# Optimization experiments

Hardware: AMD Instinct MI355X
Metric: run time of the kernel (lower is better)

The kernel has to match this reference:

```python
import jax, jax.numpy as jnp
import numpy as np

N, E = 50000, 600000
IN_C, HID, OUT_C = 256, 128, 2
R, B, L = 7, 8, 3
ALPHA = 0.1


def _rgcn(x, src, dst, etype, comp, basis, root, bias):
    # comp: [R,B], basis: [B,d,d] -> per-relation weights W: [R,d,d]
    n, d = x.shape
    W = jnp.einsum('rb,bdf->rdf', comp, basis)
    # combined (dst, relation) segment id for per-relation mean aggregation
    seg = dst * R + etype
    msg = x[src]  # [E,d] gather
    s = jax.ops.segment_sum(msg, seg, num_segments=n * R)  # [N*R,d]
    cnt = jax.ops.segment_sum(jnp.ones((E,), x.dtype), seg, num_segments=n * R)
    agg = (s / jnp.maximum(cnt, 1.0)[:, None]).reshape(n, R, d)  # per-relation mean
    return x @ root + bias + jnp.einsum('nrd,rdf->nf', agg, W)


def setup_inputs() -> dict:
    key = jax.random.key(0)
    ks = jax.random.split(key, 10)
    sc = 0.05
    x = jax.random.normal(ks[0], (N, IN_C), dtype=jnp.float32)
    edge_index = jax.random.randint(ks[1], (2, E), 0, N)
    edge_type = jax.random.randint(ks[2], (E,), 0, R)
    # GPR temp init: alpha*(1-alpha)^k, last entry (1-alpha)^K
    temp = jnp.asarray(ALPHA * (1.0 - ALPHA) ** np.arange(L + 1), dtype=jnp.float32)
    temp = temp.at[-1].set((1.0 - ALPHA) ** L)
    lin1_w = jax.random.normal(ks[3], (IN_C, HID), jnp.float32) * sc
    lin1_b = jnp.zeros((HID,), jnp.float32)
    lin2_w = jax.random.normal(ks[4], (HID, OUT_C), jnp.float32) * sc
    lin2_b = jnp.zeros((OUT_C,), jnp.float32)
    comps = jax.random.normal(ks[5], (L, R, B), jnp.float32) * sc
    bases = jax.random.normal(ks[6], (L, B, HID, HID), jnp.float32) * sc
    roots = jax.random.normal(ks[7], (L, HID, HID), jnp.float32) * sc
    conv_biases = jnp.zeros((L, HID), jnp.float32)
    return dict(x=x, edge_index=edge_index, edge_type=edge_type, temp=temp,
                lin1_w=lin1_w, lin1_b=lin1_b, lin2_w=lin2_w, lin2_b=lin2_b,
                comps=comps, bases=bases, roots=roots, conv_biases=conv_biases)


def reference(x, edge_index, edge_type, temp, lin1_w, lin1_b, lin2_w, lin2_b,
              comps, bases, roots, conv_biases):
    src, dst = edge_index[0], edge_index[1]
    h = x @ lin1_w + lin1_b
    hidden = h * temp[0]
    cur = hidden
    for i in range(L):
        cur = _rgcn(cur, src, dst, edge_type, comps[i], bases[i], roots[i], conv_biases[i])
        if i < L - 1:
            cur = jax.nn.relu(cur)  # dropout p=0.4 is identity in eval mode
        hidden = hidden + temp[i + 1] * cur
    return hidden @ lin2_w + lin2_b
```

## Files before the change

kernel.cpp:

```cpp
#include <hip/hip_runtime.h>
#include <cstdint>


constexpr int N_NODES  = 50000;
constexpr int E_EDGES  = 600000;
constexpr int R_REL    = 7;
constexpr int HID      = 128;
constexpr int IN_C     = 256;
constexpr int L_LAYERS = 3;
constexpr int AGG_COLS = 896;
constexpr int K_CAT    = 1024;
constexpr int NR       = N_NODES * R_REL;
constexpr int SCANR_BLOCKS = (NR + 255) / 256;

#define DEVI __device__ __forceinline__

using short8  = __attribute__((ext_vector_type(8))) short;
using floatx4 = __attribute__((ext_vector_type(4))) float;

DEVI unsigned short f2bf(float f) {
  unsigned u = __float_as_uint(f);
  unsigned r = (u + 0x7FFFu + ((u >> 16) & 1u)) >> 16;
  return (unsigned short)r;
}
DEVI float bf2f(unsigned short h) { return __uint_as_float(((unsigned)h) << 16); }

__global__ __launch_bounds__(256) void cast_w1_kernel(
    const float* __restrict__ w1, unsigned short* __restrict__ w1T)
{
  int t = blockIdx.x * 256 + threadIdx.x;
  if (t >= HID * IN_C) return;
  int m = t >> 8, k = t & 255;
  w1T[m * IN_C + k] = f2bf(w1[k * HID + m]);
}

__global__ __launch_bounds__(256) void build_wcat2(
    const float* __restrict__ comps,
    const float* __restrict__ bases,
    const float* __restrict__ roots,
    unsigned short* __restrict__ wcat2T)
{
  int t = blockIdx.x * 256 + threadIdx.x;
  if (t >= L_LAYERS * 128 * K_CAT) return;
  int l   = t >> 17;
  int rem = t & 131071;
  int f   = rem >> 10;
  int k   = rem & 1023;
  float v;
  if (k < 128) {
    v = roots[((size_t)l * 128 + k) * 128 + f];
  } else {
    int r = (k - 128) >> 7, d = (k - 128) & 127;
    const float* cp = comps + ((size_t)l * R_REL + r) * 8;
    const float* bp = bases + (((size_t)l * 8) * 128 + d) * 128 + f;
    float s = 0.f;
#pragma unroll
    for (int b = 0; b < 8; ++b) s += cp[b] * bp[(size_t)b * 128 * 128];
    v = s;
  }
  wcat2T[t] = f2bf(v);
}

__global__ __launch_bounds__(256) void hist_kernel(
    const int* __restrict__ ei, const int* __restrict__ et,
    int* __restrict__ cntRel)
{
  int e = blockIdx.x * 256 + threadIdx.x;
  if (e >= E_EDGES) return;
  atomicAdd(&cntRel[ei[E_EDGES + e] * R_REL + et[e]], 1);
}

__global__ __launch_bounds__(256) void scanA_kernel(
    const int* __restrict__ cnt, int* __restrict__ tmpOff,
    int* __restrict__ blockSums)
{
  __shared__ int s[256];
  int i = blockIdx.x * 256 + threadIdx.x;
  int v = (i < NR) ? cnt[i] : 0;
  s[threadIdx.x] = v;
  __syncthreads();
#pragma unroll
  for (int d = 1; d < 256; d <<= 1) {
    int t = (threadIdx.x >= d) ? s[threadIdx.x - d] : 0;
    __syncthreads();
    s[threadIdx.x] += t;
    __syncthreads();
  }
  if (i < NR) tmpOff[i] = s[threadIdx.x] - v;
  if (threadIdx.x == 255) blockSums[blockIdx.x] = s[255];
}

__global__ __launch_bounds__(256) void scanB_kernel(int* __restrict__ bs)
{
  __shared__ int s[256];
  __shared__ int carry;
  if (threadIdx.x == 0) carry = 0;
  __syncthreads();
  for (int base = 0; base < SCANR_BLOCKS; base += 256) {
    int cOld = carry;
    int i = base + threadIdx.x;
    int v = (i < SCANR_BLOCKS) ? bs[i] : 0;
    s[threadIdx.x] = v;
    __syncthreads();
#pragma unroll
    for (int d = 1; d < 256; d <<= 1) {
      int t = (threadIdx.x >= d) ? s[threadIdx.x - d] : 0;
      __syncthreads();
      s[threadIdx.x] += t;
      __syncthreads();
    }
    if (i < SCANR_BLOCKS) bs[i] = s[threadIdx.x] - v + cOld;
    __syncthreads();
    if (threadIdx.x == 0) carry = cOld + s[255];
    __syncthreads();
  }
}

__global__ __launch_bounds__(256) void scanC_kernel(
    const int* __restrict__ tmpOff, const int* __restrict__ blockSums,
    int* __restrict__ drs)
{
  int i = blockIdx.x * 256 + threadIdx.x;
  if (i < NR) drs[i] = tmpOff[i] + blockSums[blockIdx.x];
  if (i == 0) drs[NR] = E_EDGES;
}

__global__ __launch_bounds__(256) void place_kernel(
    const int* __restrict__ ei, const int* __restrict__ et,
    const int* __restrict__ drs, int* __restrict__ cursor,
    unsigned short* __restrict__ esrc)
{
  int e = blockIdx.x * 256 + threadIdx.x;
  if (e >= E_EDGES) return;
  int seg = ei[E_EDGES + e] * R_REL + et[e];
  int pos = drs[seg] + atomicAdd(&cursor[seg], 1);
  esrc[pos] = (unsigned short)ei[e];
}

__global__ __launch_bounds__(256) void agg_reg_kernel(
    const unsigned short* __restrict__ curA,
    const unsigned short* __restrict__ esrc,
    const int* __restrict__ drs,
    unsigned short* __restrict__ aggB)
{
  const int tid  = threadIdx.x;
  const int lane = tid & 63;
  const int dst  = blockIdx.x * 4 + (tid >> 6);
  if (dst >= N_NODES) return;
  const int segBase = dst * R_REL;

  int bnd = drs[segBase + (lane & 7)];
  const int a0    = __shfl(bnd, 0);
  const int total = __shfl(bnd, 7) - a0;

  int pk = 0;
  if (lane < total) pk = (int)esrc[a0 + lane];

  const unsigned* colp = (const unsigned*)curA + lane;

  int p = a0;
  int aPrev = a0;
#pragma unroll
  for (int r = 0; r < R_REL; ++r) {
    int br = __shfl(bnd, r + 1);
    float sx = 0.f, sy = 0.f;
    for (; p < br; ++p) {
      int idx = p - a0;
      int src = (idx < 64) ? __shfl(pk, idx) : (int)esrc[p];
      unsigned v = colp[src * 64];
      sx += bf2f((unsigned short)(v & 0xFFFF));
      sy += bf2f((unsigned short)(v >> 16));
    }
    int c = br - aPrev;
    float sc = (c > 0) ? 1.0f / (float)c : 0.f;
    unsigned pck = (unsigned)f2bf(sx * sc) | ((unsigned)f2bf(sy * sc) << 16);
    *(unsigned*)(aggB + (size_t)dst * AGG_COLS + r * HID + lane * 2) = pck;
    aPrev = br;
  }
}

__global__ __launch_bounds__(256) void gemm_lin1(
    const float* __restrict__ x,
    const unsigned short* __restrict__ BT,
    const float* __restrict__ bias,
    const float* __restrict__ temp,
    unsigned short* __restrict__ b0out)
{
  __shared__ unsigned short Atile[64][136];
  __shared__ unsigned short Btile[128][136];
  const int tid  = threadIdx.x;
  const int row0 = blockIdx.x * 64;
  const int lane = tid & 63;
  const int wid  = tid >> 6;
  const int wrow = (wid & 1) * 32;
  const int wcol = (wid >> 1) * 64;
  const int l15  = lane & 15;
  const int quad = lane >> 4;

  floatx4 acc[2][4] = {};

  for (int k0 = 0; k0 < IN_C; k0 += 128) {
#pragma unroll
    for (int it = 0; it < 4; ++it) {
      int chunk = it * 256 + tid;
      int r = chunk >> 4, cc = (chunk & 15) << 3;
      int grow = row0 + r;
      uint4 va = make_uint4(0u, 0u, 0u, 0u);
      if (grow < N_NODES) {
        const float* xp = x + (size_t)grow * IN_C + k0 + cc;
        float4 f0 = *(const float4*)xp;
        float4 f1 = *(const float4*)(xp + 4);
        va.x = (unsigned)f2bf(f0.x) | ((unsigned)f2bf(f0.y) << 16);
        va.y = (unsigned)f2bf(f0.z) | ((unsigned)f2bf(f0.w) << 16);
        va.z = (unsigned)f2bf(f1.x) | ((unsigned)f2bf(f1.y) << 16);
        va.w = (unsigned)f2bf(f1.z) | ((unsigned)f2bf(f1.w) << 16);
      }
      *(uint4*)(&Atile[r][cc]) = va;
    }
#pragma unroll
    for (int it = 0; it < 8; ++it) {
      int chunk = it * 256 + tid;
      int n = chunk >> 4, cc = (chunk & 15) << 3;
      *(uint4*)(&Btile[n][cc]) =
          *(const uint4*)(BT + (size_t)n * IN_C + k0 + cc);
    }
    __syncthreads();
#pragma unroll
    for (int ks = 0; ks < 4; ++ks) {
      int kc = ks * 32 + quad * 8;
      short8 af[2], bfr[4];
#pragma unroll
      for (int i = 0; i < 2; ++i)
        af[i] = *(const short8*)(&Atile[wrow + i * 16 + l15][kc]);
#pragma unroll
      for (int j = 0; j < 4; ++j)
        bfr[j] = *(const short8*)(&Btile[wcol + j * 16 + l15][kc]);
#pragma unroll
      for (int i = 0; i < 2; ++i)
#pragma unroll
        for (int j = 0; j < 4; ++j)
          acc[i][j] = __builtin_amdgcn_mfma_f32_16x16x32_bf16(
              af[i], bfr[j], acc[i][j], 0, 0, 0);
    }
    __syncthreads();
  }

  float t0 = temp[0];
#pragma unroll
  for (int i = 0; i < 2; ++i) {
    int lrow0 = wrow + i * 16 + quad * 4;
#pragma unroll
    for (int j = 0; j < 4; ++j) {
      int gcol = wcol + j * 16 + l15;
      float bb = bias[gcol];
#pragma unroll
      for (int r = 0; r < 4; ++r)
        Atile[lrow0 + r][gcol] = f2bf(t0 * (acc[i][j][r] + bb));
    }
  }
  __syncthreads();
#pragma unroll
  for (int it = 0; it < 4; ++it) {
    int chunk = it * 256 + tid;
    int r = chunk >> 4, cc = (chunk & 15) << 3;
    int grow = row0 + r;
    if (grow < N_NODES)
      *(uint4*)(b0out + (size_t)grow * HID + cc) = *(const uint4*)(&Atile[r][cc]);
  }
}

__global__ __launch_bounds__(256) void gemm_layer(
    const unsigned short* __restrict__ curA,
    const unsigned short* __restrict__ aggB,
    const unsigned short* __restrict__ BT,
    const float* __restrict__ bias,
    unsigned short* __restrict__ bout,
    int layer)
{
  __shared__ unsigned short Atile[32][136];
  __shared__ unsigned short Btile[128][136];
  const int tid  = threadIdx.x;
  const int row0 = blockIdx.x * 32;
  const int lane = tid & 63;
  const int wid  = tid >> 6;
  const int wrow = (wid & 1) * 16;
  const int wcol = (wid >> 1) * 64;
  const int l15  = lane & 15;
  const int quad = lane >> 4;

  floatx4 acc[4] = {};

  for (int p = 0; p < 8; ++p) {
#pragma unroll
    for (int it = 0; it < 8; ++it) {
      int chunk = it * 256 + tid;
      int n = chunk >> 4, cc = (chunk & 15) << 3;
      *(uint4*)(&Btile[n][cc]) =
          *(const uint4*)(BT + (size_t)n * K_CAT + p * 128 + cc);
    }
#pragma unroll
    for (int it = 0; it < 2; ++it) {
      int chunk = it * 256 + tid;
      int r = chunk >> 4, cc = (chunk & 15) << 3;
      int grow = row0 + r;
      uint4 va = make_uint4(0u, 0u, 0u, 0u);
      if (grow < N_NODES) {
        if (p == 0)
          va = *(const uint4*)(curA + (size_t)grow * HID + cc);
        else
          va = *(const uint4*)(aggB + (size_t)grow * AGG_COLS +
                               (p - 1) * 128 + cc);
      }
      *(uint4*)(&Atile[r][cc]) = va;
    }
    __syncthreads();
#pragma unroll
    for (int ks = 0; ks < 4; ++ks) {
      int kc = ks * 32 + quad * 8;
      short8 af = *(const short8*)(&Atile[wrow + l15][kc]);
      short8 bfr[4];
#pragma unroll
      for (int j = 0; j < 4; ++j)
        bfr[j] = *(const short8*)(&Btile[wcol + j * 16 + l15][kc]);
#pragma unroll
      for (int j = 0; j < 4; ++j)
        acc[j] = __builtin_amdgcn_mfma_f32_16x16x32_bf16(af, bfr[j], acc[j],
                                                         0, 0, 0);
    }
    __syncthreads();
  }

  const bool isLast = (layer == L_LAYERS - 1);
  {
    int lrow0 = wrow + quad * 4;
#pragma unroll
    for (int j = 0; j < 4; ++j) {
      int gcol = wcol + j * 16 + l15;
      float bb = bias[gcol];
#pragma unroll
      for (int r = 0; r < 4; ++r) {
        float c = acc[j][r] + bb;
        if (!isLast) c = fmaxf(c, 0.f);
        Atile[lrow0 + r][gcol] = f2bf(c);
      }
    }
  }
  __syncthreads();
#pragma unroll
  for (int it = 0; it < 2; ++it) {
    int chunk = it * 256 + tid;
    int r = chunk >> 4, cc = (chunk & 15) << 3;
    int grow = row0 + r;
    if (grow < N_NODES)
      *(uint4*)(bout + (size_t)grow * HID + cc) = *(const uint4*)(&Atile[r][cc]);
  }
}

__global__ __launch_bounds__(256) void final_kernel(
    const unsigned short* __restrict__ b0, const unsigned short* __restrict__ b1,
    const unsigned short* __restrict__ b2v, const unsigned short* __restrict__ b3,
    const float* __restrict__ temp,
    const float* __restrict__ w2, const float* __restrict__ b2bias,
    float* __restrict__ out)
{
  int node = blockIdx.x * 4 + (threadIdx.x >> 6);
  int lane = threadIdx.x & 63;
  if (node >= N_NODES) return;
  float t1 = temp[1], t2 = temp[2], t3 = temp[3];
  size_t base = (size_t)node * 64 + lane;
  unsigned u0 = ((const unsigned*)b0)[base];
  unsigned u1 = ((const unsigned*)b1)[base];
  unsigned u2 = ((const unsigned*)b2v)[base];
  unsigned u3 = ((const unsigned*)b3)[base];
  float hx = bf2f((unsigned short)(u0 & 0xFFFF)) +
             t1 * bf2f((unsigned short)(u1 & 0xFFFF)) +
             t2 * bf2f((unsigned short)(u2 & 0xFFFF)) +
             t3 * bf2f((unsigned short)(u3 & 0xFFFF));
  float hy = bf2f((unsigned short)(u0 >> 16)) +
             t1 * bf2f((unsigned short)(u1 >> 16)) +
             t2 * bf2f((unsigned short)(u2 >> 16)) +
             t3 * bf2f((unsigned short)(u3 >> 16));
  int d0 = lane * 2, d1 = lane * 2 + 1;
  float a0 = hx * w2[d0 * 2 + 0] + hy * w2[d1 * 2 + 0];
  float a1 = hx * w2[d0 * 2 + 1] + hy * w2[d1 * 2 + 1];
#pragma unroll
  for (int off = 32; off > 0; off >>= 1) {
    a0 += __shfl_down(a0, off);
    a1 += __shfl_down(a1, off);
  }
  if (lane == 0) {
    out[node * 2 + 0] = a0 + b2bias[0];
    out[node * 2 + 1] = a1 + b2bias[1];
  }
}

extern "C" void kernel_launch(void* const* d_in, const int* in_sizes, int n_in,
                              void* d_out, int out_size, void* d_ws, size_t ws_size,
                              hipStream_t stream) {
  const float* x     = (const float*)d_in[0];
  const int*   ei    = (const int*)d_in[1];
  const int*   et    = (const int*)d_in[2];
  const float* temp  = (const float*)d_in[3];
  const float* w1    = (const float*)d_in[4];
  const float* b1    = (const float*)d_in[5];
  const float* w2    = (const float*)d_in[6];
  const float* b2    = (const float*)d_in[7];
  const float* comps = (const float*)d_in[8];
  const float* bases = (const float*)d_in[9];
  const float* roots = (const float*)d_in[10];
  const float* cbias = (const float*)d_in[11];

  char* ws = (char*)d_ws;
  size_t off = 0;
  auto take = [&](size_t bytes) {
    char* p = ws + off;
    off = (off + bytes + 255) & ~(size_t)255;
    return p;
  };
  unsigned short* wcat2T = (unsigned short*)take((size_t)L_LAYERS * 128 * K_CAT * 2);
  unsigned short* w1T    = (unsigned short*)take((size_t)HID * IN_C * 2);
  int*   cntRel  = (int*)take((size_t)NR * 4);
  int*   tmpOffR = (int*)take((size_t)NR * 4);
  int*   blockSumsR = (int*)take((size_t)SCANR_BLOCKS * 4);
  int*   drs     = (int*)take((size_t)(NR + 1) * 4);
  int*   cursorR = (int*)take((size_t)NR * 4);
  unsigned short* esrc = (unsigned short*)take((size_t)E_EDGES * 2);
  unsigned short* bl[L_LAYERS + 1];
  for (int i = 0; i <= L_LAYERS; ++i)
    bl[i] = (unsigned short*)take((size_t)N_NODES * HID * 2);
  unsigned short* aggB = (unsigned short*)take((size_t)N_NODES * AGG_COLS * 2);

  hipMemsetAsync(cntRel, 0, (size_t)NR * 4, stream);
  hipMemsetAsync(cursorR, 0, (size_t)NR * 4, stream);

  hipLaunchKernelGGL(build_wcat2, dim3((L_LAYERS * 128 * K_CAT + 255) / 256),
                     dim3(256), 0, stream, comps, bases, roots, wcat2T);
  hipLaunchKernelGGL(cast_w1_kernel, dim3((HID * IN_C + 255) / 256), dim3(256),
                     0, stream, w1, w1T);
  hipLaunchKernelGGL(hist_kernel, dim3((E_EDGES + 255) / 256), dim3(256), 0,
                     stream, ei, et, cntRel);
  hipLaunchKernelGGL(scanA_kernel, dim3(SCANR_BLOCKS), dim3(256), 0, stream,
                     cntRel, tmpOffR, blockSumsR);
  hipLaunchKernelGGL(scanB_kernel, dim3(1), dim3(256), 0, stream, blockSumsR);
  hipLaunchKernelGGL(scanC_kernel, dim3(SCANR_BLOCKS), dim3(256), 0, stream,
                     tmpOffR, blockSumsR, drs);
  hipLaunchKernelGGL(place_kernel, dim3((E_EDGES + 255) / 256), dim3(256), 0,
                     stream, ei, et, drs, cursorR, esrc);

  const int rowBlocks64 = (N_NODES + 63) / 64;
  const int rowBlocks32 = (N_NODES + 31) / 32;
  hipLaunchKernelGGL(gemm_lin1, dim3(rowBlocks64), dim3(256), 0, stream,
                     x, w1T, b1, temp, bl[0]);

  for (int l = 0; l < L_LAYERS; ++l) {
    hipLaunchKernelGGL(agg_reg_kernel, dim3((N_NODES + 3) / 4), dim3(256),
                       0, stream, bl[l], esrc, drs, aggB);
    hipLaunchKernelGGL(gemm_layer, dim3(rowBlocks32), dim3(256), 0, stream,
                       bl[l], aggB, wcat2T + (size_t)l * 128 * K_CAT,
                       cbias + (size_t)l * HID, bl[l + 1], l);
  }

  hipLaunchKernelGGL(final_kernel, dim3((N_NODES + 3) / 4), dim3(256), 0, stream,
                     bl[0], bl[1], bl[2], bl[3], temp, w2, b2, (float*)d_out);
}
```

Before: 527.6 us.

## Chunk aggregation and layer GEMM over destination ranges to keep agg buffer cache-resident

Splits each layer's aggregation and GEMM into two destination-node chunks that share a smaller aggregation buffer, so the bf16 aggregate written by the gather kernel can stay in last-level cache before the GEMM reads it. The aggregation kernel also drops the wave-level shuffle preload of edge sources and segment bounds and reads them directly from global memory. The cost is twice as many kernel launches, smaller grids per launch, and more redundant esrc/drs loads per edge.

```diff
diff --git a/kernel.cpp b/kernel.cpp
--- a/kernel.cpp
+++ b/kernel.cpp
@@ -12,6 +12,7 @@
 constexpr int K_CAT    = 1024;
 constexpr int NR       = N_NODES * R_REL;
 constexpr int SCANR_BLOCKS = (NR + 255) / 256;
+constexpr int CHUNK    = 25000;
 
 #define DEVI __device__ __forceinline__
 
@@ -137,44 +138,35 @@
   esrc[pos] = (unsigned short)ei[e];
 }
 
-__global__ __launch_bounds__(256) void agg_reg_kernel(
+__global__ __launch_bounds__(256) void agg_chunk_kernel(
     const unsigned short* __restrict__ curA,
     const unsigned short* __restrict__ esrc,
     const int* __restrict__ drs,
-    unsigned short* __restrict__ aggB)
-{
-  const int tid  = threadIdx.x;
-  const int lane = tid & 63;
-  const int dst  = blockIdx.x * 4 + (tid >> 6);
-  if (dst >= N_NODES) return;
+    unsigned short* __restrict__ aggC,
+    int dstBase, int dstEnd)
+{
+  const int lane = threadIdx.x & 63;
+  const int dst  = dstBase + blockIdx.x * 4 + (threadIdx.x >> 6);
+  if (dst >= dstEnd) return;
+  const unsigned* curW = (const unsigned*)curA;
   const int segBase = dst * R_REL;
-
-  int bnd = drs[segBase + (lane & 7)];
-  const int a0    = __shfl(bnd, 0);
-  const int total = __shfl(bnd, 7) - a0;
-
-  int pk = 0;
-  if (lane < total) pk = (int)esrc[a0 + lane];
-
-  const unsigned* colp = (const unsigned*)curA + lane;
-
-  int p = a0;
-  int aPrev = a0;
+  const size_t outBase = (size_t)(dst - dstBase) * AGG_COLS;
+
+  int aPrev = drs[segBase];
 #pragma unroll
   for (int r = 0; r < R_REL; ++r) {
-    int br = __shfl(bnd, r + 1);
+    int br = drs[segBase + r + 1];
     float sx = 0.f, sy = 0.f;
-    for (; p < br; ++p) {
-      int idx = p - a0;
-      int src = (idx < 64) ? __shfl(pk, idx) : (int)esrc[p];
-      unsigned v = colp[src * 64];
+    for (int p = aPrev; p < br; ++p) {
+      int src = (int)esrc[p];
+      unsigned v = curW[(size_t)src * 64 + lane];
       sx += bf2f((unsigned short)(v & 0xFFFF));
       sy += bf2f((unsigned short)(v >> 16));
     }
     int c = br - aPrev;
     float sc = (c > 0) ? 1.0f / (float)c : 0.f;
     unsigned pck = (unsigned)f2bf(sx * sc) | ((unsigned)f2bf(sy * sc) << 16);
-    *(unsigned*)(aggB + (size_t)dst * AGG_COLS + r * HID + lane * 2) = pck;
+    *(unsigned*)(aggC + outBase + r * HID + lane * 2) = pck;
     aPrev = br;
   }
 }
@@ -271,16 +263,16 @@
 
 __global__ __launch_bounds__(256) void gemm_layer(
     const unsigned short* __restrict__ curA,
-    const unsigned short* __restrict__ aggB,
+    const unsigned short* __restrict__ aggC,
     const unsigned short* __restrict__ BT,
     const float* __restrict__ bias,
     unsigned short* __restrict__ bout,
-    int layer)
+    int layer, int dstBase, int dstEnd)
 {
   __shared__ unsigned short Atile[32][136];
   __shared__ unsigned short Btile[128][136];
   const int tid  = threadIdx.x;
-  const int row0 = blockIdx.x * 32;
+  const int row0 = dstBase + blockIdx.x * 32;
   const int lane = tid & 63;
   const int wid  = tid >> 6;
   const int wrow = (wid & 1) * 16;
@@ -304,11 +296,11 @@
       int r = chunk >> 4, cc = (chunk & 15) << 3;
       int grow = row0 + r;
       uint4 va = make_uint4(0u, 0u, 0u, 0u);
-      if (grow < N_NODES) {
+      if (grow < dstEnd) {
         if (p == 0)
           va = *(const uint4*)(curA + (size_t)grow * HID + cc);
         else
-          va = *(const uint4*)(aggB + (size_t)grow * AGG_COLS +
+          va = *(const uint4*)(aggC + (size_t)(grow - dstBase) * AGG_COLS +
                                (p - 1) * 128 + cc);
       }
       *(uint4*)(&Atile[r][cc]) = va;
@@ -351,7 +343,7 @@
     int chunk = it * 256 + tid;
     int r = chunk >> 4, cc = (chunk & 15) << 3;
     int grow = row0 + r;
-    if (grow < N_NODES)
+    if (grow < dstEnd)
       *(uint4*)(bout + (size_t)grow * HID + cc) = *(const uint4*)(&Atile[r][cc]);
   }
 }
@@ -428,7 +420,7 @@
   unsigned short* bl[L_LAYERS + 1];
   for (int i = 0; i <= L_LAYERS; ++i)
     bl[i] = (unsigned short*)take((size_t)N_NODES * HID * 2);
-  unsigned short* aggB = (unsigned short*)take((size_t)N_NODES * AGG_COLS * 2);
+  unsigned short* aggC = (unsigned short*)take((size_t)CHUNK * AGG_COLS * 2);
 
   hipMemsetAsync(cntRel, 0, (size_t)NR * 4, stream);
   hipMemsetAsync(cursorR, 0, (size_t)NR * 4, stream);
@@ -448,16 +440,19 @@
                      stream, ei, et, drs, cursorR, esrc);
 
   const int rowBlocks64 = (N_NODES + 63) / 64;
-  const int rowBlocks32 = (N_NODES + 31) / 32;
   hipLaunchKernelGGL(gemm_lin1, dim3(rowBlocks64), dim3(256), 0, stream,
                      x, w1T, b1, temp, bl[0]);
 
   for (int l = 0; l < L_LAYERS; ++l) {
-    hipLaunchKernelGGL(agg_reg_kernel, dim3((N_NODES + 3) / 4), dim3(256),
-                       0, stream, bl[l], esrc, drs, aggB);
-    hipLaunchKernelGGL(gemm_layer, dim3(rowBlocks32), dim3(256), 0, stream,
-                       bl[l], aggB, wcat2T + (size_t)l * 128 * K_CAT,
-                       cbias + (size_t)l * HID, bl[l + 1], l);
+    for (int c0 = 0; c0 < N_NODES; c0 += CHUNK) {
+      int cEnd = (c0 + CHUNK < N_NODES) ? (c0 + CHUNK) : N_NODES;
+      int nc = cEnd - c0;
+      hipLaunchKernelGGL(agg_chunk_kernel, dim3((nc + 3) / 4), dim3(256),
+                         0, stream, bl[l], esrc, drs, aggC, c0, cEnd);
+      hipLaunchKernelGGL(gemm_layer, dim3((nc + 31) / 32), dim3(256), 0, stream,
+                         bl[l], aggC, wcat2T + (size_t)l * 128 * K_CAT,
+                         cbias + (size_t)l * HID, bl[l + 1], l, c0, cEnd);
+    }
   }
 
   hipLaunchKernelGGL(final_kernel, dim3((N_NODES + 3) / 4), dim3(256), 0, stream,
```

After: 636.4 us. 20.6% more time.

## Fuse per-relation aggregation into layer GEMM with pre-swizzled MFMA weight fragments

Applied to the files above, without the earlier changes.

Merges the aggregation kernel and the layer GEMM into one kernel. Each block aggregates 16 destination nodes straight into a shared-memory A tile of width 1024, then runs MFMA against a weight matrix that build_wcat3 stores in per-lane fragment order, so B operands are read directly from global memory with no shared-memory staging. This removes the write and re-read of the large N×896 aggregation buffer and one launch per layer. In exchange each block does serial gathers before any compute, and every block re-reads the full weight fragments from global memory or cache.

```diff
diff --git a/kernel.cpp b/kernel.cpp
--- a/kernel.cpp
+++ b/kernel.cpp
@@ -8,10 +8,10 @@
 constexpr int HID      = 128;
 constexpr int IN_C     = 256;
 constexpr int L_LAYERS = 3;
-constexpr int AGG_COLS = 896;
 constexpr int K_CAT    = 1024;
 constexpr int NR       = N_NODES * R_REL;
 constexpr int SCANR_BLOCKS = (NR + 255) / 256;
+constexpr int AROW     = 1032;
 
 #define DEVI __device__ __forceinline__
 
@@ -34,31 +34,36 @@
   w1T[m * IN_C + k] = f2bf(w1[k * HID + m]);
 }
 
-__global__ __launch_bounds__(256) void build_wcat2(
+__global__ __launch_bounds__(256) void build_wcat3(
     const float* __restrict__ comps,
     const float* __restrict__ bases,
     const float* __restrict__ roots,
-    unsigned short* __restrict__ wcat2T)
+    unsigned short* __restrict__ wcat3)
 {
   int t = blockIdx.x * 256 + threadIdx.x;
   if (t >= L_LAYERS * 128 * K_CAT) return;
-  int l   = t >> 17;
-  int rem = t & 131071;
-  int f   = rem >> 10;
-  int k   = rem & 1023;
+  int l    = t >> 17;
+  int rem  = t & 131071;
+  int e    = rem & 7;
+  int lane = (rem >> 3) & 63;
+  int j    = (rem >> 9) & 7;
+  int ks   = (rem >> 12) & 3;
+  int p    = (rem >> 14) & 7;
+  int n = j * 16 + (lane & 15);
+  int k = p * 128 + ks * 32 + (lane >> 4) * 8 + e;
   float v;
   if (k < 128) {
-    v = roots[((size_t)l * 128 + k) * 128 + f];
+    v = roots[((size_t)l * 128 + k) * 128 + n];
   } else {
     int r = (k - 128) >> 7, d = (k - 128) & 127;
     const float* cp = comps + ((size_t)l * R_REL + r) * 8;
-    const float* bp = bases + (((size_t)l * 8) * 128 + d) * 128 + f;
+    const float* bp = bases + (((size_t)l * 8) * 128 + d) * 128 + n;
     float s = 0.f;
 #pragma unroll
     for (int b = 0; b < 8; ++b) s += cp[b] * bp[(size_t)b * 128 * 128];
     v = s;
   }
-  wcat2T[t] = f2bf(v);
+  wcat3[t] = f2bf(v);
 }
 
 __global__ __launch_bounds__(256) void hist_kernel(
@@ -135,48 +140,6 @@
   int seg = ei[E_EDGES + e] * R_REL + et[e];
   int pos = drs[seg] + atomicAdd(&cursor[seg], 1);
   esrc[pos] = (unsigned short)ei[e];
-}
-
-__global__ __launch_bounds__(256) void agg_reg_kernel(
-    const unsigned short* __restrict__ curA,
-    const unsigned short* __restrict__ esrc,
-    const int* __restrict__ drs,
-    unsigned short* __restrict__ aggB)
-{
-  const int tid  = threadIdx.x;
-  const int lane = tid & 63;
-  const int dst  = blockIdx.x * 4 + (tid >> 6);
-  if (dst >= N_NODES) return;
-  const int segBase = dst * R_REL;
-
-  int bnd = drs[segBase + (lane & 7)];
-  const int a0    = __shfl(bnd, 0);
-  const int total = __shfl(bnd, 7) - a0;
-
-  int pk = 0;
-  if (lane < total) pk = (int)esrc[a0 + lane];
-
-  const unsigned* colp = (const unsigned*)curA + lane;
-
-  int p = a0;
-  int aPrev = a0;
-#pragma unroll
-  for (int r = 0; r < R_REL; ++r) {
-    int br = __shfl(bnd, r + 1);
-    float sx = 0.f, sy = 0.f;
-    for (; p < br; ++p) {
-      int idx = p - a0;
-      int src = (idx < 64) ? __shfl(pk, idx) : (int)esrc[p];
-      unsigned v = colp[src * 64];
-      sx += bf2f((unsigned short)(v & 0xFFFF));
-      sy += bf2f((unsigned short)(v >> 16));
-    }
-    int c = br - aPrev;
-    float sc = (c > 0) ? 1.0f / (float)c : 0.f;
-    unsigned pck = (unsigned)f2bf(sx * sc) | ((unsigned)f2bf(sy * sc) << 16);
-    *(unsigned*)(aggB + (size_t)dst * AGG_COLS + r * HID + lane * 2) = pck;
-    aPrev = br;
-  }
 }
 
 __global__ __launch_bounds__(256) void gemm_lin1(
@@ -269,88 +232,94 @@
   }
 }
 
-__global__ __launch_bounds__(256) void gemm_layer(
+__global__ __launch_bounds__(256) void rgcn_block(
     const unsigned short* __restrict__ curA,
-    const unsigned short* __restrict__ aggB,
-    const unsigned short* __restrict__ BT,
+    const unsigned short* __restrict__ esrc,
+    const int* __restrict__ drs,
+    const unsigned short* __restrict__ Bfrag,
     const float* __restrict__ bias,
     unsigned short* __restrict__ bout,
     int layer)
 {
-  __shared__ unsigned short Atile[32][136];
-  __shared__ unsigned short Btile[128][136];
+  __shared__ unsigned short Atile[16][AROW];
   const int tid  = threadIdx.x;
-  const int row0 = blockIdx.x * 32;
   const int lane = tid & 63;
   const int wid  = tid >> 6;
-  const int wrow = (wid & 1) * 16;
-  const int wcol = (wid >> 1) * 64;
   const int l15  = lane & 15;
   const int quad = lane >> 4;
-
-  floatx4 acc[4] = {};
-
+  const int dst0 = blockIdx.x * 16;
+  const unsigned* curW = (const unsigned*)curA;
+
+  for (int i = 0; i < 4; ++i) {
+    int dl  = wid * 4 + i;
+    int dst = dst0 + dl;
+    if (dst < N_NODES) {
+      *(unsigned*)(&Atile[dl][lane * 2]) = curW[(size_t)dst * 64 + lane];
+      const int segBase = dst * R_REL;
+      int bnd = drs[segBase + (lane & 7)];
+      const int a0    = __shfl(bnd, 0);
+      const int total = __shfl(bnd, 7) - a0;
+      int pk = 0;
+      if (lane < total) pk = (int)esrc[a0 + lane];
+      int p = a0, aPrev = a0;
+#pragma unroll
+      for (int r = 0; r < R_REL; ++r) {
+        int br = __shfl(bnd, r + 1);
+        float sx = 0.f, sy = 0.f;
+        for (; p < br; ++p) {
+          int idx = p - a0;
+          int src = (idx < 64) ? __shfl(pk, idx) : (int)esrc[p];
+          unsigned v = curW[(size_t)src * 64 + lane];
+          sx += bf2f((unsigned short)(v & 0xFFFF));
+          sy += bf2f((unsigned short)(v >> 16));
+        }
+        int c = br - aPrev;
+        float sc = (c > 0) ? 1.0f / (float)c : 0.f;
+        unsigned pck = (unsigned)f2bf(sx * sc) | ((unsigned)f2bf(sy * sc) << 16);
+        *(unsigned*)(&Atile[dl][128 + r * HID + lane * 2]) = pck;
+        aPrev = br;
+      }
+    } else {
+#pragma unroll
+      for (int c = 0; c < 8; ++c)
+        *(unsigned*)(&Atile[dl][c * 128 + lane * 2]) = 0u;
+    }
+  }
+  __syncthreads();
+
+  floatx4 acc[2] = {};
   for (int p = 0; p < 8; ++p) {
 #pragma unroll
-    for (int it = 0; it < 8; ++it) {
-      int chunk = it * 256 + tid;
-      int n = chunk >> 4, cc = (chunk & 15) << 3;
-      *(uint4*)(&Btile[n][cc]) =
-          *(const uint4*)(BT + (size_t)n * K_CAT + p * 128 + cc);
-    }
-#pragma unroll
-    for (int it = 0; it < 2; ++it) {
-      int chunk = it * 256 + tid;
-      int r = chunk >> 4, cc = (chunk & 15) << 3;
-      int grow = row0 + r;
-      uint4 va = make_uint4(0u, 0u, 0u, 0u);
-      if (grow < N_NODES) {
-        if (p == 0)
-          va = *(const uint4*)(curA + (size_t)grow * HID + cc);
-        else
-          va = *(const uint4*)(aggB + (size_t)grow * AGG_COLS +
-                               (p - 1) * 128 + cc);
+    for (int ks = 0; ks < 4; ++ks) {
+      short8 af = *(const short8*)(&Atile[l15][p * 128 + ks * 32 + quad * 8]);
+#pragma unroll
+      for (int j = 0; j < 2; ++j) {
+        const short8 bfr = *(const short8*)(
+            Bfrag + ((((size_t)(p * 4 + ks) * 8) + (wid * 2 + j)) * 64 + lane) * 8);
+        acc[j] = __builtin_amdgcn_mfma_f32_16x16x32_bf16(af, bfr, acc[j],
+                                                         0, 0, 0);
       }
-      *(uint4*)(&Atile[r][cc]) = va;
-    }
-    __syncthreads();
-#pragma unroll
-    for (int ks = 0; ks < 4; ++ks) {
-      int kc = ks * 32 + quad * 8;
-      short8 af = *(const short8*)(&Atile[wrow + l15][kc]);
-      short8 bfr[4];
-#pragma unroll
-      for (int j = 0; j < 4; ++j)
-        bfr[j] = *(const short8*)(&Btile[wcol + j * 16 + l15][kc]);
-#pragma unroll
-      for (int j = 0; j < 4; ++j)
-        acc[j] = __builtin_amdgcn_mfma_f32_16x16x32_bf16(af, bfr[j], acc[j],
-                                                         0, 0, 0);
-    }
-    __syncthreads();
-  }
-
+    }
+  }
+
+  __syncthreads();
   const bool isLast = (layer == L_LAYERS - 1);
+  const int lrow0 = quad * 4;
+#pragma unroll
+  for (int j = 0; j < 2; ++j) {
+    int gcol = wid * 32 + j * 16 + l15;
+    float bb = bias[gcol];
+#pragma unroll
+    for (int r = 0; r < 4; ++r) {
+      float c = acc[j][r] + bb;
+      if (!isLast) c = fmaxf(c, 0.f);
+      Atile[lrow0 + r][gcol] = f2bf(c);
+    }
+  }
+  __syncthreads();
   {
-    int lrow0 = wrow + quad * 4;
-#pragma unroll
-    for (int j = 0; j < 4; ++j) {
-      int gcol = wcol + j * 16 + l15;
-      float bb = bias[gcol];
-#pragma unroll
-      for (int r = 0; r < 4; ++r) {
-        float c = acc[j][r] + bb;
-        if (!isLast) c = fmaxf(c, 0.f);
-        Atile[lrow0 + r][gcol] = f2bf(c);
-      }
-    }
-  }
-  __syncthreads();
-#pragma unroll
-  for (int it = 0; it < 2; ++it) {
-    int chunk = it * 256 + tid;
-    int r = chunk >> 4, cc = (chunk & 15) << 3;
-    int grow = row0 + r;
+    int r = tid >> 4, cc = (tid & 15) << 3;
+    int grow = dst0 + r;
     if (grow < N_NODES)
       *(uint4*)(bout + (size_t)grow * HID + cc) = *(const uint4*)(&Atile[r][cc]);
   }
@@ -417,8 +386,8 @@
     off = (off + bytes + 255) & ~(size_t)255;
     return p;
   };
-  unsigned short* wcat2T = (unsigned short*)take((size_t)L_LAYERS * 128 * K_CAT * 2);
-  unsigned short* w1T    = (unsigned short*)take((size_t)HID * IN_C * 2);
+  unsigned short* wcat3 = (unsigned short*)take((size_t)L_LAYERS * 128 * K_CAT * 2);
+  unsigned short* w1T   = (unsigned short*)take((size_t)HID * IN_C * 2);
   int*   cntRel  = (int*)take((size_t)NR * 4);
   int*   tmpOffR = (int*)take((size_t)NR * 4);
   int*   blockSumsR = (int*)take((size_t)SCANR_BLOCKS * 4);
@@ -428,13 +397,12 @@
   unsigned short* bl[L_LAYERS + 1];
   for (int i = 0; i <= L_LAYERS; ++i)
     bl[i] = (unsigned short*)take((size_t)N_NODES * HID * 2);
-  unsigned short* aggB = (unsigned short*)take((size_t)N_NODES * AGG_COLS * 2);
 
   hipMemsetAsync(cntRel, 0, (size_t)NR * 4, stream);
   hipMemsetAsync(cursorR, 0, (size_t)NR * 4, stream);
 
-  hipLaunchKernelGGL(build_wcat2, dim3((L_LAYERS * 128 * K_CAT + 255) / 256),
-                     dim3(256), 0, stream, comps, bases, roots, wcat2T);
+  hipLaunchKernelGGL(build_wcat3, dim3((L_LAYERS * 128 * K_CAT + 255) / 256),
+                     dim3(256), 0, stream, comps, bases, roots, wcat3);
   hipLaunchKernelGGL(cast_w1_kernel, dim3((HID * IN_C + 255) / 256), dim3(256),
                      0, stream, w1, w1T);
   hipLaunchKernelGGL(hist_kernel, dim3((E_EDGES + 255) / 256), dim3(256), 0,
@@ -448,15 +416,13 @@
                      stream, ei, et, drs, cursorR, esrc);
 
   const int rowBlocks64 = (N_NODES + 63) / 64;
-  const int rowBlocks32 = (N_NODES + 31) / 32;
   hipLaunchKernelGGL(gemm_lin1, dim3(rowBlocks64), dim3(256), 0, stream,
                      x, w1T, b1, temp, bl[0]);
 
+  const int fusedBlocks = (N_NODES + 15) / 16;
   for (int l = 0; l < L_LAYERS; ++l) {
-    hipLaunchKernelGGL(agg_reg_kernel, dim3((N_NODES + 3) / 4), dim3(256),
-                       0, stream, bl[l], esrc, drs, aggB);
-    hipLaunchKernelGGL(gemm_layer, dim3(rowBlocks32), dim3(256), 0, stream,
-                       bl[l], aggB, wcat2T + (size_t)l * 128 * K_CAT,
+    hipLaunchKernelGGL(rgcn_block, dim3(fusedBlocks), dim3(256), 0, stream,
+                       bl[l], esrc, drs, wcat3 + (size_t)l * 128 * K_CAT,
                        cbias + (size_t)l * HID, bl[l + 1], l);
   }
 
```

Result: slower. 547.7 us (+3.8%).
